# Kernel optimization log

Hardware: AMD Instinct MI355X
Metric: run time of the kernel (lower is better)

## Reference

```python
import jax, jax.numpy as jnp
import numpy as np

HIDDEN = 4096
N_HEADS = 32
N_KV_HEADS = 8
HEAD_DIM = HIDDEN // N_HEADS          # 128
GROUP = N_HEADS // N_KV_HEADS         # 4 q-heads per kv-head
Q_SIZE = N_HEADS * HEAD_DIM           # 4096
KV_SIZE = N_KV_HEADS * HEAD_DIM       # 1024
T = 2048


def setup_inputs() -> dict:
    key = jax.random.key(0)
    k1, k2, k3 = jax.random.split(key, 3)
    positions = jnp.arange(T, dtype=jnp.int64) if jax.config.jax_enable_x64 else jnp.arange(T, dtype=jnp.int32)
    hidden_states = jax.random.normal(k1, (T, HIDDEN), dtype=jnp.float32)
    # torch.nn.Linear weights: out = x @ W.T
    w_qkv = jax.random.normal(k2, (Q_SIZE + 2 * KV_SIZE, HIDDEN), dtype=jnp.float32) * 0.02
    w_o = jax.random.normal(k3, (HIDDEN, HIDDEN), dtype=jnp.float32) * 0.02
    return {"positions": positions, "hidden_states": hidden_states, "w_qkv": w_qkv, "w_o": w_o}


def reference(positions, hidden_states, w_qkv, w_o):
    del positions  # rotary is a no-op in the fake module
    t = hidden_states.shape[0]
    scaling = HEAD_DIM ** -0.5

    qkv = hidden_states @ w_qkv.T                              # [T, q+2kv]
    q, k, v = jnp.split(qkv, [Q_SIZE, Q_SIZE + KV_SIZE], axis=-1)
    # GQA mapping: q-head h uses kv-head h // GROUP (contiguous groups)
    q = q.reshape(t, N_KV_HEADS, GROUP, HEAD_DIM)              # [T, Hkv, G, d]
    k = k.reshape(t, N_KV_HEADS, HEAD_DIM)                     # [T, Hkv, d]
    v = v.reshape(t, N_KV_HEADS, HEAD_DIM)

    # Cache starts empty -> token i attends to keys 0..i (causal prefill)
    logits = jnp.einsum('tkgd,skd->kgts', q, k) * scaling      # [Hkv, G, T, T]
    causal = jnp.tril(jnp.ones((t, t), dtype=bool))            # s <= t
    logits = jnp.where(causal, logits, jnp.finfo(logits.dtype).min)
    weights = jax.nn.softmax(logits, axis=-1)
    ctx = jnp.einsum('kgts,skd->tkgd', weights, v)             # [T, Hkv, G, d]
    ctx = ctx.reshape(t, HIDDEN)
    return ctx @ w_o.T
```

## Files before the change

### kernel.cpp

```cpp
#include <hip/hip_runtime.h>

typedef unsigned short u16;
typedef __bf16 bf16x8 __attribute__((ext_vector_type(8)));
typedef float f32x4 __attribute__((ext_vector_type(4)));

__device__ __forceinline__ u16 f2bf(float f) {
  union { float f; unsigned u; } v; v.f = f;
  unsigned r = v.u + 0x7FFFu + ((v.u >> 16) & 1u);
  return (u16)(r >> 16);
}

__device__ __forceinline__ u16 bfc(float f) {
  __bf16 h = (__bf16)f;
  return *(u16*)&h;
}

__device__ __forceinline__ void gload16(const void* g, void* l) {
  __builtin_amdgcn_global_load_lds(
      (const __attribute__((address_space(1))) unsigned int*)g,
      (__attribute__((address_space(3))) unsigned int*)l, 16, 0, 0);
}

__global__ __launch_bounds__(256) void cvt_bf16(const float* __restrict__ in,
                                                u16* __restrict__ out, long n) {
  long i = ((long)blockIdx.x * 256 + threadIdx.x) * 8;
  const long stride = (long)gridDim.x * 2048;
  for (; i < n; i += stride) {
    float4 a = *(const float4*)(in + i);
    float4 b = *(const float4*)(in + i + 4);
    uint4 o;
    o.x = (unsigned)f2bf(a.x) | ((unsigned)f2bf(a.y) << 16);
    o.y = (unsigned)f2bf(a.z) | ((unsigned)f2bf(a.w) << 16);
    o.z = (unsigned)f2bf(b.x) | ((unsigned)f2bf(b.y) << 16);
    o.w = (unsigned)f2bf(b.z) | ((unsigned)f2bf(b.w) << 16);
    *(uint4*)(out + i) = o;
  }
}

__global__ __launch_bounds__(256) void pack_b(const float* __restrict__ w,
                                              u16* __restrict__ out, int kb32) {
  const int tid = threadIdx.x;
  const int unit = blockIdx.x * 4 + (tid >> 6);
  const int ln = tid & 63, lr = ln & 15, lg = ln >> 4;
  const int n16 = unit / kb32, k32 = unit % kb32;
  const float* src = w + (size_t)(n16 * 16 + lr) * (kb32 * 32) + k32 * 32 + lg * 8;
  float4 a = *(const float4*)src;
  float4 b = *(const float4*)(src + 4);
  uint4 o;
  o.x = (unsigned)f2bf(a.x) | ((unsigned)f2bf(a.y) << 16);
  o.y = (unsigned)f2bf(a.z) | ((unsigned)f2bf(a.w) << 16);
  o.z = (unsigned)f2bf(b.x) | ((unsigned)f2bf(b.y) << 16);
  o.w = (unsigned)f2bf(b.z) | ((unsigned)f2bf(b.w) << 16);
  *(uint4*)(out + (size_t)unit * 512 + ln * 8) = o;
}

template <int BN, typename OUT>
__global__ __launch_bounds__(256) void gemmV(const u16* __restrict__ A,
                                             const u16* __restrict__ Bp,
                                             OUT* __restrict__ C,
                                             int M, int N, int K) {
  constexpr int BM = 128;
  constexpr int MREP = 4;
  constexpr int NREP = BN / 32;
  constexpr int AI = 4;
  __shared__ __align__(16) u16 sA[2][BM * 64];

  const int tid = threadIdx.x;
  const int w = tid >> 6, ln = tid & 63;
  const int lr = ln & 15, lg = ln >> 4;
  const int wr = w >> 1, wc = w & 1;

  const int nN = N / BN;
  const int bm = ((int)blockIdx.x / nN) * BM;
  const int bn = ((int)blockIdx.x % nN) * BN;

  const int srow = tid >> 3;
  const int scol = (((tid & 7) * 16) ^ ((srow & 7) << 4)) >> 1;
  const u16* pA = A + (size_t)(bm + srow) * K + scol;

  const int mask = (lr & 7) << 4;
  const int pAr = (wr * 64 + lr) * 128;
  const int kb32 = K >> 5;
  const u16* pB = Bp + ((size_t)((bn >> 4) + wc * NREP)) * kb32 * 512 + ln * 8;

  f32x4 acc[MREP][NREP] = {};
  const int nk = K >> 6;

  auto stageA = [&](int buf, int t) {
    const int k0 = t << 6;
#pragma unroll
    for (int i = 0; i < AI; ++i)
      gload16(pA + (size_t)i * 32 * K + k0, (char*)sA[buf] + i * 4096 + tid * 16);
  };
  auto loadB = [&](bf16x8 (&br)[NREP][2], int t) {
#pragma unroll
    for (int nf = 0; nf < NREP; ++nf)
#pragma unroll
      for (int s = 0; s < 2; ++s)
        br[nf][s] = *(const bf16x8*)(pB + ((size_t)nf * kb32 + 2 * t + s) * 512);
  };

  bf16x8 b[NREP][2];
  stageA(0, 0);
  loadB(b, 0);

#pragma unroll 1
  for (int t = 0; t < nk; ++t) {
    const int buf = t & 1;
    const char* lA = (const char*)sA[buf];
    const bool more = (t + 1 < nk);

    asm volatile("s_waitcnt vmcnt(0)" ::: "memory");
    __builtin_amdgcn_sched_barrier(0);
    __builtin_amdgcn_s_barrier();
    __builtin_amdgcn_sched_barrier(0);
    if (more) stageA(buf ^ 1, t + 1);

    bf16x8 af[MREP][2];
#pragma unroll
    for (int m = 0; m < MREP; ++m)
      af[m][0] = *(const bf16x8*)(lA + pAr + m * 2048 + ((lg * 16) ^ mask));
#pragma unroll
    for (int m = 0; m < MREP; ++m)
      af[m][1] = *(const bf16x8*)(lA + pAr + m * 2048 + ((lg * 16 + 64) ^ mask));

    asm volatile("s_waitcnt lgkmcnt(%0)" :: "n"(MREP) : "memory");
    __builtin_amdgcn_sched_barrier(0);
    __builtin_amdgcn_s_setprio(1);
#pragma unroll
    for (int m = 0; m < MREP; ++m)
#pragma unroll
      for (int nf = 0; nf < NREP; ++nf)
        acc[m][nf] = __builtin_amdgcn_mfma_f32_16x16x32_bf16(
            af[m][0], b[nf][0], acc[m][nf], 0, 0, 0);
    __builtin_amdgcn_s_setprio(0);
    asm volatile("s_waitcnt lgkmcnt(0)" ::: "memory");
    __builtin_amdgcn_sched_barrier(0);
    __builtin_amdgcn_s_setprio(1);
#pragma unroll
    for (int m = 0; m < MREP; ++m)
#pragma unroll
      for (int nf = 0; nf < NREP; ++nf)
        acc[m][nf] = __builtin_amdgcn_mfma_f32_16x16x32_bf16(
            af[m][1], b[nf][1], acc[m][nf], 0, 0, 0);
    __builtin_amdgcn_s_setprio(0);

    if (more) loadB(b, t + 1);
  }

#pragma unroll
  for (int m = 0; m < MREP; ++m)
#pragma unroll
    for (int nf = 0; nf < NREP; ++nf)
#pragma unroll
      for (int r = 0; r < 4; ++r) {
        const int row = bm + wr * 64 + m * 16 + lg * 4 + r;
        const int col = bn + wc * (BN / 2) + nf * 16 + lr;
        const float v = acc[m][nf][r];
        if constexpr (sizeof(OUT) == 2)
          C[(size_t)row * N + col] = (OUT)bfc(v);
        else
          C[(size_t)row * N + col] = v;
      }
}

__global__ __launch_bounds__(256) void vtrans(const u16* __restrict__ qkv,
                                              u16* __restrict__ vT) {
  __shared__ u16 tile[128][65];
  const int hk = blockIdx.y;
  const int tb = blockIdx.x * 64;
  const int tid = threadIdx.x;
#pragma unroll
  for (int p = 0; p < 4; ++p) {
    const int tr = p * 16 + (tid >> 4);
    const int d0 = (tid & 15) * 8;
    const uint4 x = *(const uint4*)(qkv + (size_t)(tb + tr) * 6144 + 5120 + hk * 128 + d0);
    const u16* xv = (const u16*)&x;
#pragma unroll
    for (int j = 0; j < 8; ++j) tile[d0 + j][tr] = xv[j];
  }
  __syncthreads();
#pragma unroll
  for (int p = 0; p < 4; ++p) {
    const int d = p * 32 + (tid >> 3);
    const int t0 = (tid & 7) * 8;
    u16 v[8];
#pragma unroll
    for (int j = 0; j < 8; ++j) v[j] = tile[d][t0 + j];
    uint4 o;
    unsigned* ov = (unsigned*)&o;
#pragma unroll
    for (int j = 0; j < 4; ++j)
      ov[j] = (unsigned)v[2 * j] | ((unsigned)v[2 * j + 1] << 16);
    *(uint4*)(vT + (size_t)hk * 128 * 2048 + (size_t)d * 2048 + tb + t0) = o;
  }
}

__global__ __launch_bounds__(256) void attn(const u16* __restrict__ qkv,
                                            const u16* __restrict__ vT,
                                            u16* __restrict__ ctx) {
  __shared__ __align__(16) u16 sK[2][64 * 128];
  __shared__ __align__(16) u16 sV[2][128 * 64];
  __shared__ __align__(16) u16 sP[4 * 16 * 64];
  const int tid = threadIdx.x, w = tid >> 6, ln = tid & 63;
  const int lr = ln & 15, lg = ln >> 4;
  const int h = blockIdx.y, hk = h >> 2;
  const int pi = blockIdx.x;

  const float Cs = 0.12751737f;
  char* const pw = (char*)sP + w * 2048;

  auto stage = [&](int buf, int kt) {
    const int kvbase = kt * 64;
#pragma unroll
    for (int i = 0; i < 4; ++i) {
      const int off = i * 4096 + tid * 16;
      {
        const int row = off >> 8, cbp = off & 255;
        const int cb = cbp ^ ((row & 7) << 4);
        gload16(qkv + (size_t)(kvbase + row) * 6144 + 4096 + hk * 128 + (cb >> 1),
                (char*)sK + buf * 16384 + off);
      }
      {
        const int row = off >> 7, cbp = off & 127;
        const int cb = cbp ^ ((row & 7) << 4);
        gload16(vT + (size_t)hk * 262144 + (size_t)row * 2048 + kvbase + (cb >> 1),
                (char*)sV + buf * 16384 + off);
      }
    }
  };

#pragma unroll 1
  for (int ph = 0; ph < 2; ++ph) {
    const int qt = ph ? (31 - pi) : pi;
    const int qbase = qt * 64;
    const int nkt = qt + 1;

    bf16x8 qf[4];
    {
      const u16* qrow = qkv + (size_t)(qbase + w * 16 + lr) * 6144 + h * 128 + lg * 8;
#pragma unroll
      for (int kk = 0; kk < 4; ++kk) qf[kk] = *(const bf16x8*)(qrow + kk * 32);
    }

    f32x4 acc_o[8] = {};
    float l_p[4] = {0.f, 0.f, 0.f, 0.f};

    stage(0, 0);

#pragma unroll 1
    for (int kt = 0; kt < nkt; ++kt) {
      const int buf = kt & 1;
      const int kvbase = kt * 64;
      __syncthreads();
      if (kt + 1 < nkt) stage(buf ^ 1, kt + 1);

      char* const kbase = (char*)sK + buf * 16384;
      char* const vbase = (char*)sV + buf * 16384;

      f32x4 sacc[4] = {};
#pragma unroll
      for (int kk = 0; kk < 4; ++kk) {
#pragma unroll
        for (int nf = 0; nf < 4; ++nf) {
          const int row = nf * 16 + lr;
          const int byt = row * 256 + ((kk * 64 + lg * 16) ^ ((row & 7) << 4));
          const bf16x8 kf = *(const bf16x8*)(kbase + byt);
          sacc[nf] = __builtin_amdgcn_mfma_f32_16x16x32_bf16(qf[kk], kf, sacc[nf], 0, 0, 0);
        }
      }

      const bool diag = (kt == qt);
      float p[4][4];
#pragma unroll
      for (int r = 0; r < 4; ++r) {
        const int qrow = qbase + w * 16 + lg * 4 + r;
        float rs = 0.f;
#pragma unroll
        for (int nf = 0; nf < 4; ++nf) {
          const bool masked = diag && (kvbase + nf * 16 + lr > qrow);
          const float e = masked ? 0.f : exp2f(sacc[nf][r] * Cs);
          p[nf][r] = e;
          rs += e;
        }
        l_p[r] += rs;
      }

#pragma unroll
      for (int r = 0; r < 4; ++r) {
        const int row = lg * 4 + r;
#pragma unroll
        for (int nf = 0; nf < 4; ++nf) {
          const int col = nf * 16 + lr;
          const int byt = row * 128 + ((2 * col) ^ ((row & 7) << 4));
          *(u16*)(pw + byt) = bfc(p[nf][r]);
        }
      }

#pragma unroll
      for (int kk2 = 0; kk2 < 2; ++kk2) {
        const int pbyt = lr * 128 + ((kk2 * 64 + lg * 16) ^ ((lr & 7) << 4));
        const bf16x8 pf = *(const bf16x8*)(pw + pbyt);
#pragma unroll
        for (int o = 0; o < 8; ++o) {
          const int vrow = o * 16 + lr;
          const int vbyt = vrow * 128 + ((kk2 * 64 + lg * 16) ^ ((vrow & 7) << 4));
          const bf16x8 vf = *(const bf16x8*)(vbase + vbyt);
          acc_o[o] = __builtin_amdgcn_mfma_f32_16x16x32_bf16(pf, vf, acc_o[o], 0, 0, 0);
        }
      }
    }

#pragma unroll
    for (int r = 0; r < 4; ++r) {
      float l = l_p[r];
      l += __shfl_xor(l, 1);
      l += __shfl_xor(l, 2);
      l += __shfl_xor(l, 4);
      l += __shfl_xor(l, 8);
      const float inv = 1.f / l;
      const int t = qbase + w * 16 + lg * 4 + r;
#pragma unroll
      for (int o = 0; o < 8; ++o)
        ctx[(size_t)t * 4096 + h * 128 + o * 16 + lr] = bfc(acc_o[o][r] * inv);
    }
    __syncthreads();
  }
}

extern "C" void kernel_launch(void* const* d_in, const int* in_sizes, int n_in,
                              void* d_out, int out_size, void* d_ws, size_t ws_size,
                              hipStream_t stream) {
  (void)in_sizes; (void)n_in; (void)out_size; (void)ws_size;
  const float* hidden = (const float*)d_in[1];
  const float* w_qkv = (const float*)d_in[2];
  const float* w_o = (const float*)d_in[3];
  float* out = (float*)d_out;
  char* ws = (char*)d_ws;

  u16* xb    = (u16*)(ws + 0);
  u16* wqkvp = (u16*)(ws + 16777216);
  u16* wop   = (u16*)(ws + 67108864);
  u16* qkvb  = (u16*)(ws + 100663296);
  u16* vTb   = (u16*)(ws + 125829120);
  u16* ctxb  = (u16*)(ws + 130023424);

  cvt_bf16<<<4096, 256, 0, stream>>>(hidden, xb, (long)2048 * 4096);
  pack_b<<<12288, 256, 0, stream>>>(w_qkv, wqkvp, 128);
  pack_b<<<8192, 256, 0, stream>>>(w_o, wop, 128);
  gemmV<96, u16><<<1024, 256, 0, stream>>>(xb, wqkvp, qkvb, 2048, 6144, 4096);
  vtrans<<<dim3(32, 8), 256, 0, stream>>>(qkvb, vTb);
  attn<<<dim3(16, 32), 256, 0, stream>>>(qkvb, vTb, ctxb);
  gemmV<128, float><<<512, 256, 0, stream>>>(ctxb, wop, out, 2048, 4096, 4096);
}
```

Baseline: 353.8 us.

## Fuse w_o bf16 conversion into output GEMM and widen QKV GEMM tile

The output projection GEMM now reads the fp32 w_o weights directly, converts them to bf16 in registers and feeds the MFMAs. This removes the separate pack_b launch and its 64MB write plus read round trip. The QKV GEMM tile width goes from 96 to 192 columns, halving its grid and reusing each A tile across more columns. The risks are more register pressure from the fp32 staging (bx/by) and the wider NREP, and strided uncoalesced fp32 B loads issued from every block, so the weights are re-read once per M-tile.

```diff
diff --git a/kernel.cpp b/kernel.cpp
--- a/kernel.cpp
+++ b/kernel.cpp
@@ -54,9 +54,9 @@
   *(uint4*)(out + (size_t)unit * 512 + ln * 8) = o;
 }
 
-template <int BN, typename OUT>
+template <int BN, typename OUT, bool F32B>
 __global__ __launch_bounds__(256) void gemmV(const u16* __restrict__ A,
-                                             const u16* __restrict__ Bp,
+                                             const void* __restrict__ Bsrc,
                                              OUT* __restrict__ C,
                                              int M, int N, int K) {
   constexpr int BM = 128;
@@ -81,9 +81,14 @@
   const int mask = (lr & 7) << 4;
   const int pAr = (wr * 64 + lr) * 128;
   const int kb32 = K >> 5;
-  const u16* pB = Bp + ((size_t)((bn >> 4) + wc * NREP)) * kb32 * 512 + ln * 8;
+  const u16* pB = (const u16*)Bsrc +
+                  ((size_t)((bn >> 4) + wc * NREP)) * kb32 * 512 + ln * 8;
+  const float* pBf = (const float*)Bsrc +
+                     (size_t)(bn + wc * NREP * 16 + lr) * K + lg * 8;
 
   f32x4 acc[MREP][NREP] = {};
+  bf16x8 b[NREP][2];
+  f32x4 bx[NREP][2], by[NREP][2];
   const int nk = K >> 6;
 
   auto stageA = [&](int buf, int t) {
@@ -92,17 +97,39 @@
     for (int i = 0; i < AI; ++i)
       gload16(pA + (size_t)i * 32 * K + k0, (char*)sA[buf] + i * 4096 + tid * 16);
   };
-  auto loadB = [&](bf16x8 (&br)[NREP][2], int t) {
+  auto loadBpk = [&](int t) {
 #pragma unroll
     for (int nf = 0; nf < NREP; ++nf)
 #pragma unroll
       for (int s = 0; s < 2; ++s)
-        br[nf][s] = *(const bf16x8*)(pB + ((size_t)nf * kb32 + 2 * t + s) * 512);
-  };
-
-  bf16x8 b[NREP][2];
+        b[nf][s] = *(const bf16x8*)(pB + ((size_t)nf * kb32 + 2 * t + s) * 512);
+  };
+  auto issueB = [&](int t) {
+#pragma unroll
+    for (int nf = 0; nf < NREP; ++nf)
+#pragma unroll
+      for (int s = 0; s < 2; ++s) {
+        const float* src = pBf + (size_t)nf * 16 * K + t * 64 + s * 32;
+        bx[nf][s] = *(const f32x4*)src;
+        by[nf][s] = *(const f32x4*)(src + 4);
+      }
+  };
+  auto cvtB = [&]() {
+#pragma unroll
+    for (int nf = 0; nf < NREP; ++nf)
+#pragma unroll
+      for (int s = 0; s < 2; ++s) {
+        bf16x8 r;
+#pragma unroll
+        for (int j = 0; j < 4; ++j) r[j] = (__bf16)bx[nf][s][j];
+#pragma unroll
+        for (int j = 0; j < 4; ++j) r[4 + j] = (__bf16)by[nf][s][j];
+        b[nf][s] = r;
+      }
+  };
+
   stageA(0, 0);
-  loadB(b, 0);
+  if constexpr (F32B) issueB(0); else loadBpk(0);
 
 #pragma unroll 1
   for (int t = 0; t < nk; ++t) {
@@ -115,6 +142,10 @@
     __builtin_amdgcn_s_barrier();
     __builtin_amdgcn_sched_barrier(0);
     if (more) stageA(buf ^ 1, t + 1);
+    if constexpr (F32B) {
+      cvtB();
+      if (more) issueB(t + 1);
+    }
 
     bf16x8 af[MREP][2];
 #pragma unroll
@@ -145,7 +176,7 @@
             af[m][1], b[nf][1], acc[m][nf], 0, 0, 0);
     __builtin_amdgcn_s_setprio(0);
 
-    if (more) loadB(b, t + 1);
+    if constexpr (!F32B) { if (more) loadBpk(t + 1); }
   }
 
 #pragma unroll
@@ -340,16 +371,14 @@
 
   u16* xb    = (u16*)(ws + 0);
   u16* wqkvp = (u16*)(ws + 16777216);
-  u16* wop   = (u16*)(ws + 67108864);
   u16* qkvb  = (u16*)(ws + 100663296);
   u16* vTb   = (u16*)(ws + 125829120);
   u16* ctxb  = (u16*)(ws + 130023424);
 
   cvt_bf16<<<4096, 256, 0, stream>>>(hidden, xb, (long)2048 * 4096);
   pack_b<<<12288, 256, 0, stream>>>(w_qkv, wqkvp, 128);
-  pack_b<<<8192, 256, 0, stream>>>(w_o, wop, 128);
-  gemmV<96, u16><<<1024, 256, 0, stream>>>(xb, wqkvp, qkvb, 2048, 6144, 4096);
+  gemmV<192, u16, false><<<512, 256, 0, stream>>>(xb, wqkvp, qkvb, 2048, 6144, 4096);
   vtrans<<<dim3(32, 8), 256, 0, stream>>>(qkvb, vTb);
   attn<<<dim3(16, 32), 256, 0, stream>>>(qkvb, vTb, ctxb);
-  gemmV<128, float><<<512, 256, 0, stream>>>(ctxb, wop, out, 2048, 4096, 4096);
-}
+  gemmV<128, float, true><<<512, 256, 0, stream>>>(ctxb, w_o, out, 2048, 4096, 4096);
+}
```

After: 487.0 us. 37.7% more time.
